# Optimization experiments

Measured on AMD Instinct MI355X. Metric: run time of the kernel, lower is better.

Reference implementation:

```python
import jax, jax.numpy as jnp
import numpy as np

N_LAYER = 3

def setup_inputs() -> dict:
    key = jax.random.key(0)
    k1, k2 = jax.random.split(key)
    N, D, E = 100000, 128, 1600000
    x = jax.random.normal(k1, (N, D), dtype=jnp.float32)
    edge_index = jax.random.randint(k2, (2, E), 0, N, dtype=jnp.int64)
    return {"x": x, "edge_index": edge_index}

def reference(x, edge_index):
    # SimpleConv(aggr='mean', combine_root='self_loop'):
    # add self-loops, then mean-aggregate source features into targets.
    # norm=None -> identity. keep_init=True -> return [x, h1, ..., hL].
    n = x.shape[0]
    src, dst = edge_index[0], edge_index[1]
    # degree of each target node (self-loop adds +1)
    deg = jax.ops.segment_sum(jnp.ones(src.shape[0], dtype=x.dtype), dst, num_segments=n)
    inv_deg = 1.0 / (deg + 1.0)  # [N]
    outs = [x]
    h = x
    for _ in range(N_LAYER):
        agg = jax.ops.segment_sum(h[src], dst, num_segments=n)  # [N, D]
        h = (agg + h) * inv_deg[:, None]  # mean over neighbors + self
        outs.append(h)
    return jnp.stack(outs)  # [n_layer+1, N, D]
```

## Files before the change

kernel.cpp:

```cpp
#include <hip/hip_runtime.h>
#include <hip/hip_fp16.h>

#ifndef MIN
#define MIN(a,b) ((a)<(b)?(a):(b))
#endif

#define BSHIFT 9
#define NB1 256
#define TILE 4096
#define B4CAP 12288

typedef float floatx2 __attribute__((ext_vector_type(2)));

#if defined(__has_builtin)
#if __has_builtin(__builtin_amdgcn_cvt_pk_f32_fp8) && __has_builtin(__builtin_amdgcn_cvt_pk_fp8_f32)
#define HW_FP8 1
#endif
#endif

template <bool HI>
__device__ __forceinline__ floatx2 fp8x2_dec_word(unsigned w) {
#ifdef HW_FP8
    return __builtin_amdgcn_cvt_pk_f32_fp8((int)w, HI);
#else
    unsigned v = HI ? (w >> 16) : w;
    floatx2 r;
    unsigned b0 = v & 0xFFu, b1 = (v >> 8) & 0xFFu;
    float f0 = __uint_as_float(((b0 & 0x80u) << 24) | ((b0 & 0x7Fu) << 20));
    float f1 = __uint_as_float(((b1 & 0x80u) << 24) | ((b1 & 0x7Fu) << 20));
    r.x = f0 * 1.329227995784916e+36f;
    r.y = f1 * 1.329227995784916e+36f;
    return r;
#endif
}

__device__ __forceinline__ unsigned short fp8x2_enc(float x, float y) {
#ifdef HW_FP8
    int p = __builtin_amdgcn_cvt_pk_fp8_f32(x, y, 0, false);
    return (unsigned short)((unsigned)p & 0xFFFFu);
#else
    auto enc1 = [](float f) -> unsigned {
        float yv = f * 7.52316384526264e-37f;
        unsigned u = __float_as_uint(yv);
        unsigned s = (u >> 24) & 0x80u;
        unsigned em = u & 0x7FFFFFFFu;
        unsigned keep = em >> 20;
        unsigned rem = em & 0xFFFFFu;
        keep += (rem > 0x80000u || (rem == 0x80000u && (keep & 1u))) ? 1u : 0u;
        if (keep > 0x7Fu) keep = 0x7Fu;
        return s | keep;
    };
    return (unsigned short)(enc1(x) | (enc1(y) << 8));
#endif
}

__global__ void __launch_bounds__(256) k_hist(const int* __restrict__ dst, int E,
                                              unsigned* __restrict__ partial) {
    __shared__ unsigned c[256];
    int t = threadIdx.x;
    c[t] = 0;
    __syncthreads();
    int i = blockIdx.x * blockDim.x + t;
    int stride = gridDim.x * blockDim.x;
    for (; i < E; i += stride) atomicAdd(&c[((unsigned)dst[i]) >> BSHIFT], 1);
    __syncthreads();
    partial[blockIdx.x * 256 + t] = c[t];
}

__global__ void __launch_bounds__(256) k_bscan(const unsigned* __restrict__ partial,
                                               int K, unsigned* __restrict__ bcnt,
                                               unsigned* __restrict__ bbase,
                                               unsigned* __restrict__ gcur,
                                               int* __restrict__ offs, int N, int E) {
    __shared__ unsigned sm[256];
    int t = threadIdx.x;
    unsigned s = 0;
    if (t < K)
        for (int blk = 0; blk < NB1; ++blk) s += partial[blk * 256 + t];
    sm[t] = (t < K) ? s : 0;
    __syncthreads();
    unsigned v = sm[t];
    for (int off = 1; off < 256; off <<= 1) {
        unsigned x = (t >= off) ? sm[t - off] : 0;
        __syncthreads();
        sm[t] += x;
        __syncthreads();
    }
    unsigned excl = sm[t] - v;
    if (t < K) {
        bcnt[t] = s;
        bbase[t] = excl;
        gcur[t] = excl;
    }
    if (t == 0) offs[N] = E;
}

__global__ void __launch_bounds__(256) k_split(const int* __restrict__ src,
                                               const int* __restrict__ dst, int E,
                                               unsigned* __restrict__ gcur,
                                               uint2* __restrict__ pairs) {
    __shared__ uint2 sp[TILE];
    __shared__ unsigned cnt[256], sscan[256], gb[256];
    int t = threadIdx.x;
    int base = blockIdx.x * TILE;
    cnt[t] = 0;
    __syncthreads();

    unsigned pk[TILE / 256];
    #pragma unroll
    for (int j = 0; j < TILE / 256; ++j) {
        int i = base + j * 256 + t;
        if (i < E) {
            unsigned b = ((unsigned)dst[i]) >> BSHIFT;
            unsigned r = atomicAdd(&cnt[b], 1);
            pk[j] = (b << 16) | r;
        } else {
            pk[j] = 0xFFFFFFFFu;
        }
    }
    __syncthreads();

    unsigned v = cnt[t];
    sscan[t] = v;
    __syncthreads();
    for (int off = 1; off < 256; off <<= 1) {
        unsigned x = (t >= off) ? sscan[t - off] : 0;
        __syncthreads();
        sscan[t] += x;
        __syncthreads();
    }
    sscan[t] -= v;
    __syncthreads();

    #pragma unroll
    for (int j = 0; j < TILE / 256; ++j) {
        if (pk[j] != 0xFFFFFFFFu) {
            int i = base + j * 256 + t;
            unsigned b = pk[j] >> 16, r = pk[j] & 0xFFFFu;
            sp[sscan[b] + r] = make_uint2((unsigned)src[i], (unsigned)dst[i]);
        }
    }
    __syncthreads();

    unsigned n = cnt[t];
    gb[t] = n ? atomicAdd(&gcur[t], n) : 0u;
    __syncthreads();

    int cntTile = MIN(TILE, E - base);
    #pragma unroll
    for (int j = 0; j < TILE / 256; ++j) {
        int p = j * 256 + t;
        if (p < cntTile) {
            uint2 e = sp[p];
            unsigned b = e.y >> BSHIFT;
            pairs[gb[b] + (unsigned)p - sscan[b]] = e;
        }
    }
}

__global__ void __launch_bounds__(512) k_csr(const uint2* __restrict__ pairs,
                                             const unsigned* __restrict__ bcnt,
                                             const unsigned* __restrict__ bbase,
                                             int* __restrict__ adj,
                                             int* __restrict__ offs, int N) {
    __shared__ unsigned adjL[B4CAP];
    __shared__ unsigned cnt[512], cnt2[512], sc[512];
    int t = threadIdx.x;
    int b = blockIdx.x;
    unsigned nb = bcnt[b];
    unsigned bb = bbase[b];
    cnt[t] = 0;
    cnt2[t] = 0;
    __syncthreads();

    for (unsigned i = t; i < nb; i += 512)
        atomicAdd(&cnt[pairs[bb + i].y & 511u], 1);
    __syncthreads();

    unsigned v = cnt[t];
    sc[t] = v;
    __syncthreads();
    for (int off = 1; off < 512; off <<= 1) {
        unsigned x = (t >= off) ? sc[t - off] : 0;
        __syncthreads();
        sc[t] += x;
        __syncthreads();
    }
    sc[t] -= v;
    __syncthreads();

    int node = (b << BSHIFT) + t;
    if (node < N) offs[node] = (int)(bb + sc[t]);

    if (nb <= B4CAP) {
        for (unsigned i = t; i < nb; i += 512) {
            uint2 e = pairs[bb + i];
            unsigned dl = e.y & 511u;
            unsigned pos = sc[dl] + atomicAdd(&cnt2[dl], 1);
            adjL[pos] = e.x;
        }
        __syncthreads();
        for (unsigned i = t; i < nb; i += 512) adj[bb + i] = (int)adjL[i];
    } else {
        for (unsigned i = t; i < nb; i += 512) {
            uint2 e = pairs[bb + i];
            unsigned dl = e.y & 511u;
            unsigned pos = sc[dl] + atomicAdd(&cnt2[dl], 1);
            adj[bb + pos] = (int)e.x;
        }
    }
}

__global__ void k_init(const float2* __restrict__ x2, float2* __restrict__ out2,
                       unsigned short* __restrict__ t8, int n2) {
    int i = blockIdx.x * blockDim.x + threadIdx.x;
    int stride = gridDim.x * blockDim.x;
    for (; i < n2; i += stride) {
        float2 v = x2[i];
        out2[i] = v;
        t8[i] = fp8x2_enc(v.x, v.y);
    }
}

__global__ void __launch_bounds__(256) k_layer(
        const unsigned short* __restrict__ hin, float2* __restrict__ hout,
        unsigned short* __restrict__ tout, const int* __restrict__ adj,
        const int* __restrict__ offs, int N) {
    int wave = (blockIdx.x * blockDim.x + threadIdx.x) >> 6;
    int lane = threadIdx.x & 63;
    if (wave >= N) return;
    const int node = __builtin_amdgcn_readfirstlane(wave);
    const int beg = offs[node];
    const int end = offs[node + 1];

    floatx2 sf = fp8x2_dec_word<false>((unsigned)hin[(size_t)node * 64 + lane]);
    float ax = sf.x, ay = sf.y;
    float bx = 0.f, by = 0.f;

    int e = beg;
    for (; e + 16 <= end; e += 16) {
        const int* __restrict__ a = adj + __builtin_amdgcn_readfirstlane(e);
        int s[16];
        #pragma unroll
        for (int j = 0; j < 16; ++j) s[j] = a[j];
        unsigned short v[16];
        #pragma unroll
        for (int j = 0; j < 16; ++j) v[j] = hin[(size_t)s[j] * 64 + lane];
        #pragma unroll
        for (int j = 0; j < 16; j += 2) {
            floatx2 f0 = fp8x2_dec_word<false>((unsigned)v[j]);
            floatx2 f1 = fp8x2_dec_word<false>((unsigned)v[j + 1]);
            ax += f0.x; ay += f0.y;
            bx += f1.x; by += f1.y;
        }
    }
    for (; e + 8 <= end; e += 8) {
        const int* __restrict__ a = adj + __builtin_amdgcn_readfirstlane(e);
        int s[8];
        #pragma unroll
        for (int j = 0; j < 8; ++j) s[j] = a[j];
        unsigned short v[8];
        #pragma unroll
        for (int j = 0; j < 8; ++j) v[j] = hin[(size_t)s[j] * 64 + lane];
        #pragma unroll
        for (int j = 0; j < 8; j += 2) {
            floatx2 f0 = fp8x2_dec_word<false>((unsigned)v[j]);
            floatx2 f1 = fp8x2_dec_word<false>((unsigned)v[j + 1]);
            ax += f0.x; ay += f0.y;
            bx += f1.x; by += f1.y;
        }
    }
    for (; e + 2 <= end; e += 2) {
        const int* __restrict__ a = adj + __builtin_amdgcn_readfirstlane(e);
        int s0 = a[0], s1 = a[1];
        floatx2 f0 = fp8x2_dec_word<false>((unsigned)hin[(size_t)s0 * 64 + lane]);
        floatx2 f1 = fp8x2_dec_word<false>((unsigned)hin[(size_t)s1 * 64 + lane]);
        ax += f0.x; ay += f0.y;
        bx += f1.x; by += f1.y;
    }
    if (e < end) {
        int s0 = *(adj + __builtin_amdgcn_readfirstlane(e));
        floatx2 f = fp8x2_dec_word<false>((unsigned)hin[(size_t)s0 * 64 + lane]);
        ax += f.x; ay += f.y;
    }

    const float w = 1.0f / (float)(end - beg + 1);
    float2 r;
    r.x = (ax + bx) * w;
    r.y = (ay + by) * w;
    hout[(size_t)node * 64 + lane] = r;
    if (tout) tout[(size_t)node * 64 + lane] = fp8x2_enc(r.x, r.y);
}

extern "C" void kernel_launch(void* const* d_in, const int* in_sizes, int n_in,
                              void* d_out, int out_size, void* d_ws, size_t ws_size,
                              hipStream_t stream) {
    const float* x = (const float*)d_in[0];
    const int* ei = (const int*)d_in[1];
    const int N = in_sizes[0] / 128;
    const int E = in_sizes[1] / 2;
    const int* src = ei;
    const int* dst = ei + E;
    float* out = (float*)d_out;
    const int K = (N + 511) >> BSHIFT;

    char* ws = (char*)d_ws;
    size_t off = 0;
    auto carve = [&](size_t bytes) {
        void* p = ws + off;
        off = (off + bytes + 255) & ~(size_t)255;
        return p;
    };
    unsigned* partial = (unsigned*)carve((size_t)NB1 * 256 * 4);
    unsigned* bcnt    = (unsigned*)carve(256 * 4);
    unsigned* bbase   = (unsigned*)carve(256 * 4);
    unsigned* gcur    = (unsigned*)carve(256 * 4);
    int*      offs    = (int*)carve(((size_t)N + 1) * 4);
    uint2*    pairs   = (uint2*)carve((size_t)E * 8);
    int*      adj     = (int*)carve((size_t)E * 4);
    unsigned short* tab0 = (unsigned short*)carve((size_t)N * 64 * 2);
    unsigned short* tab1 = (unsigned short*)carve((size_t)N * 64 * 2);

    k_hist<<<NB1, 256, 0, stream>>>(dst, E, partial);
    k_bscan<<<1, 256, 0, stream>>>(partial, K, bcnt, bbase, gcur, offs, N, E);
    k_split<<<(E + TILE - 1) / TILE, 256, 0, stream>>>(src, dst, E, gcur, pairs);
    k_csr<<<K, 512, 0, stream>>>(pairs, bcnt, bbase, adj, offs, N);

    const int n2 = N * 64;
    k_init<<<MIN((n2 + 255) / 256, 2048), 256, 0, stream>>>(
        (const float2*)x, (float2*)out, tab0, n2);

    const size_t layer_sz = (size_t)N * 128;
    unsigned short* tabs[2] = { tab0, tab1 };
    for (int l = 1; l <= 3; ++l) {
        float* hout = out + (size_t)l * layer_sz;
        unsigned short* tin = tabs[(l - 1) & 1];
        unsigned short* tnext = (l < 3) ? tabs[l & 1] : (unsigned short*)nullptr;
        k_layer<<<(N + 3) / 4, 256, 0, stream>>>(tin, (float2*)hout, tnext, adj, offs, N);
    }
}
```

Baseline: 205.5 us.

## Use finer CSR buckets and nontemporal stores for fp32 outputs

Halves the bucket width of the two-pass radix CSR build from 512 to 256 nodes, doubling the bucket count to 391 so the k_csr stage launches more blocks. The histogram, scan and split kernels widen to 512 threads and the split tile doubles to cover more buckets. Separately, the fp32 output writes in the init and layer kernels become nontemporal stores, so the streaming output is meant to stay out of the cache that holds the gathered fp8 feature tables. The trade-off is larger per-block scans and more partial counts, and the local-memory path in k_csr now caps at a smaller per-bucket edge count.

Result: faster. 181.6 us (-11.6%).

```diff
diff --git a/kernel.cpp b/kernel.cpp
--- a/kernel.cpp
+++ b/kernel.cpp
@@ -5,10 +5,11 @@
 #define MIN(a,b) ((a)<(b)?(a):(b))
 #endif
 
-#define BSHIFT 9
+#define BSHIFT 8
+#define NBKT 512
 #define NB1 256
-#define TILE 4096
-#define B4CAP 12288
+#define TILE 8192
+#define B4CAP 6144
 
 typedef float floatx2 __attribute__((ext_vector_type(2)));
 
@@ -54,9 +55,15 @@
 #endif
 }
 
-__global__ void __launch_bounds__(256) k_hist(const int* __restrict__ dst, int E,
+__device__ __forceinline__ void nt_store_f2(float2* p, float2 v) {
+    union { double d; float2 f; } u;
+    u.f = v;
+    __builtin_nontemporal_store(u.d, (double*)p);
+}
+
+__global__ void __launch_bounds__(512) k_hist(const int* __restrict__ dst, int E,
                                               unsigned* __restrict__ partial) {
-    __shared__ unsigned c[256];
+    __shared__ unsigned c[NBKT];
     int t = threadIdx.x;
     c[t] = 0;
     __syncthreads();
@@ -64,23 +71,23 @@
     int stride = gridDim.x * blockDim.x;
     for (; i < E; i += stride) atomicAdd(&c[((unsigned)dst[i]) >> BSHIFT], 1);
     __syncthreads();
-    partial[blockIdx.x * 256 + t] = c[t];
-}
-
-__global__ void __launch_bounds__(256) k_bscan(const unsigned* __restrict__ partial,
+    partial[blockIdx.x * NBKT + t] = c[t];
+}
+
+__global__ void __launch_bounds__(512) k_bscan(const unsigned* __restrict__ partial,
                                                int K, unsigned* __restrict__ bcnt,
                                                unsigned* __restrict__ bbase,
                                                unsigned* __restrict__ gcur,
                                                int* __restrict__ offs, int N, int E) {
-    __shared__ unsigned sm[256];
+    __shared__ unsigned sm[NBKT];
     int t = threadIdx.x;
     unsigned s = 0;
     if (t < K)
-        for (int blk = 0; blk < NB1; ++blk) s += partial[blk * 256 + t];
+        for (int blk = 0; blk < NB1; ++blk) s += partial[blk * NBKT + t];
     sm[t] = (t < K) ? s : 0;
     __syncthreads();
     unsigned v = sm[t];
-    for (int off = 1; off < 256; off <<= 1) {
+    for (int off = 1; off < NBKT; off <<= 1) {
         unsigned x = (t >= off) ? sm[t - off] : 0;
         __syncthreads();
         sm[t] += x;
@@ -95,25 +102,25 @@
     if (t == 0) offs[N] = E;
 }
 
-__global__ void __launch_bounds__(256) k_split(const int* __restrict__ src,
+__global__ void __launch_bounds__(512) k_split(const int* __restrict__ src,
                                                const int* __restrict__ dst, int E,
                                                unsigned* __restrict__ gcur,
                                                uint2* __restrict__ pairs) {
     __shared__ uint2 sp[TILE];
-    __shared__ unsigned cnt[256], sscan[256], gb[256];
+    __shared__ unsigned cnt[NBKT], sscan[NBKT], gb[NBKT];
     int t = threadIdx.x;
     int base = blockIdx.x * TILE;
     cnt[t] = 0;
     __syncthreads();
 
-    unsigned pk[TILE / 256];
+    unsigned pk[TILE / 512];
     #pragma unroll
-    for (int j = 0; j < TILE / 256; ++j) {
-        int i = base + j * 256 + t;
+    for (int j = 0; j < TILE / 512; ++j) {
+        int i = base + j * 512 + t;
         if (i < E) {
             unsigned b = ((unsigned)dst[i]) >> BSHIFT;
             unsigned r = atomicAdd(&cnt[b], 1);
-            pk[j] = (b << 16) | r;
+            pk[j] = (b << 13) | r;
         } else {
             pk[j] = 0xFFFFFFFFu;
         }
@@ -123,7 +130,7 @@
     unsigned v = cnt[t];
     sscan[t] = v;
     __syncthreads();
-    for (int off = 1; off < 256; off <<= 1) {
+    for (int off = 1; off < NBKT; off <<= 1) {
         unsigned x = (t >= off) ? sscan[t - off] : 0;
         __syncthreads();
         sscan[t] += x;
@@ -133,10 +140,10 @@
     __syncthreads();
 
     #pragma unroll
-    for (int j = 0; j < TILE / 256; ++j) {
+    for (int j = 0; j < TILE / 512; ++j) {
         if (pk[j] != 0xFFFFFFFFu) {
-            int i = base + j * 256 + t;
-            unsigned b = pk[j] >> 16, r = pk[j] & 0xFFFFu;
+            int i = base + j * 512 + t;
+            unsigned b = pk[j] >> 13, r = pk[j] & 8191u;
             sp[sscan[b] + r] = make_uint2((unsigned)src[i], (unsigned)dst[i]);
         }
     }
@@ -148,8 +155,8 @@
 
     int cntTile = MIN(TILE, E - base);
     #pragma unroll
-    for (int j = 0; j < TILE / 256; ++j) {
-        int p = j * 256 + t;
+    for (int j = 0; j < TILE / 512; ++j) {
+        int p = j * 512 + t;
         if (p < cntTile) {
             uint2 e = sp[p];
             unsigned b = e.y >> BSHIFT;
@@ -164,38 +171,38 @@
                                              int* __restrict__ adj,
                                              int* __restrict__ offs, int N) {
     __shared__ unsigned adjL[B4CAP];
-    __shared__ unsigned cnt[512], cnt2[512], sc[512];
+    __shared__ unsigned cnt[256], cnt2[256], sc[256];
     int t = threadIdx.x;
     int b = blockIdx.x;
     unsigned nb = bcnt[b];
     unsigned bb = bbase[b];
-    cnt[t] = 0;
-    cnt2[t] = 0;
+    if (t < 256) { cnt[t] = 0; cnt2[t] = 0; }
     __syncthreads();
 
     for (unsigned i = t; i < nb; i += 512)
-        atomicAdd(&cnt[pairs[bb + i].y & 511u], 1);
-    __syncthreads();
-
-    unsigned v = cnt[t];
-    sc[t] = v;
-    __syncthreads();
-    for (int off = 1; off < 512; off <<= 1) {
-        unsigned x = (t >= off) ? sc[t - off] : 0;
-        __syncthreads();
-        sc[t] += x;
-        __syncthreads();
-    }
-    sc[t] -= v;
+        atomicAdd(&cnt[pairs[bb + i].y & 255u], 1);
+    __syncthreads();
+
+    unsigned v = 0;
+    if (t < 256) { v = cnt[t]; sc[t] = v; }
+    __syncthreads();
+    for (int off = 1; off < 256; off <<= 1) {
+        unsigned x = 0;
+        if (t < 256 && t >= off) x = sc[t - off];
+        __syncthreads();
+        if (t < 256) sc[t] += x;
+        __syncthreads();
+    }
+    if (t < 256) sc[t] -= v;
     __syncthreads();
 
     int node = (b << BSHIFT) + t;
-    if (node < N) offs[node] = (int)(bb + sc[t]);
+    if (t < 256 && node < N) offs[node] = (int)(bb + sc[t]);
 
     if (nb <= B4CAP) {
         for (unsigned i = t; i < nb; i += 512) {
             uint2 e = pairs[bb + i];
-            unsigned dl = e.y & 511u;
+            unsigned dl = e.y & 255u;
             unsigned pos = sc[dl] + atomicAdd(&cnt2[dl], 1);
             adjL[pos] = e.x;
         }
@@ -204,7 +211,7 @@
     } else {
         for (unsigned i = t; i < nb; i += 512) {
             uint2 e = pairs[bb + i];
-            unsigned dl = e.y & 511u;
+            unsigned dl = e.y & 255u;
             unsigned pos = sc[dl] + atomicAdd(&cnt2[dl], 1);
             adj[bb + pos] = (int)e.x;
         }
@@ -217,7 +224,7 @@
     int stride = gridDim.x * blockDim.x;
     for (; i < n2; i += stride) {
         float2 v = x2[i];
-        out2[i] = v;
+        nt_store_f2(&out2[i], v);
         t8[i] = fp8x2_enc(v.x, v.y);
     }
 }
@@ -288,7 +295,7 @@
     float2 r;
     r.x = (ax + bx) * w;
     r.y = (ay + by) * w;
-    hout[(size_t)node * 64 + lane] = r;
+    nt_store_f2(&hout[(size_t)node * 64 + lane], r);
     if (tout) tout[(size_t)node * 64 + lane] = fp8x2_enc(r.x, r.y);
 }
 
@@ -302,7 +309,7 @@
     const int* src = ei;
     const int* dst = ei + E;
     float* out = (float*)d_out;
-    const int K = (N + 511) >> BSHIFT;
+    const int K = (N + 255) >> BSHIFT;
 
     char* ws = (char*)d_ws;
     size_t off = 0;
@@ -311,19 +318,19 @@
         off = (off + bytes + 255) & ~(size_t)255;
         return p;
     };
-    unsigned* partial = (unsigned*)carve((size_t)NB1 * 256 * 4);
-    unsigned* bcnt    = (unsigned*)carve(256 * 4);
-    unsigned* bbase   = (unsigned*)carve(256 * 4);
-    unsigned* gcur    = (unsigned*)carve(256 * 4);
+    unsigned* partial = (unsigned*)carve((size_t)NB1 * NBKT * 4);
+    unsigned* bcnt    = (unsigned*)carve(NBKT * 4);
+    unsigned* bbase   = (unsigned*)carve(NBKT * 4);
+    unsigned* gcur    = (unsigned*)carve(NBKT * 4);
     int*      offs    = (int*)carve(((size_t)N + 1) * 4);
     uint2*    pairs   = (uint2*)carve((size_t)E * 8);
     int*      adj     = (int*)carve((size_t)E * 4);
     unsigned short* tab0 = (unsigned short*)carve((size_t)N * 64 * 2);
     unsigned short* tab1 = (unsigned short*)carve((size_t)N * 64 * 2);
 
-    k_hist<<<NB1, 256, 0, stream>>>(dst, E, partial);
-    k_bscan<<<1, 256, 0, stream>>>(partial, K, bcnt, bbase, gcur, offs, N, E);
-    k_split<<<(E + TILE - 1) / TILE, 256, 0, stream>>>(src, dst, E, gcur, pairs);
+    k_hist<<<NB1, 512, 0, stream>>>(dst, E, partial);
+    k_bscan<<<1, NBKT, 0, stream>>>(partial, K, bcnt, bbase, gcur, offs, N, E);
+    k_split<<<(E + TILE - 1) / TILE, 512, 0, stream>>>(src, dst, E, gcur, pairs);
     k_csr<<<K, 512, 0, stream>>>(pairs, bcnt, bbase, adj, offs, N);
 
     const int n2 = N * 64;
```
